# Kernel tuning notes

Measured on AMD Instinct MI355X. Metric: run time of the kernel, lower is better.

## Reference

```python
import jax, jax.numpy as jnp
import numpy as np

EMB = 1024
HEADS = 16
HEADSIZE = EMB // HEADS
EPS = 1e-5  # torch LayerNorm default


def _layernorm(x, g, b):
    # normalize over last dim (headsize)
    m = jnp.mean(x, axis=-1, keepdims=True)
    v = jnp.mean((x - m) ** 2, axis=-1, keepdims=True)
    return (x - m) * jax.lax.rsqrt(v + EPS) * g + b


def setup_inputs() -> dict:
    key = jax.random.key(0)
    ks = jax.random.split(key, 6)
    B, T = 4, 2048
    s = 1.0 / np.sqrt(EMB)  # ~ torch Linear init scale
    return {
        "x": jax.random.normal(ks[0], (B, T, EMB), dtype=jnp.float32),
        "Wk": jax.random.normal(ks[1], (EMB, EMB), dtype=jnp.float32) * s,
        "Wq": jax.random.normal(ks[2], (EMB, EMB), dtype=jnp.float32) * s,
        "Wv": jax.random.normal(ks[3], (EMB, EMB), dtype=jnp.float32) * s,
        "Wo": jax.random.normal(ks[4], (EMB, EMB), dtype=jnp.float32) * s,
        "bo": jnp.zeros((EMB,), dtype=jnp.float32),
        "kln_g": jnp.ones((HEADSIZE,), dtype=jnp.float32),
        "kln_b": jnp.zeros((HEADSIZE,), dtype=jnp.float32),
        "qln_g": jnp.ones((HEADSIZE,), dtype=jnp.float32),
        "qln_b": jnp.zeros((HEADSIZE,), dtype=jnp.float32),
    }


def reference(x, Wk, Wq, Wv, Wo, bo, kln_g, kln_b, qln_g, qln_b):
    B, T, E = x.shape
    # projections (torch Linear: y = x @ W.T), split into heads
    k = jnp.einsum("bte,fe->btf", x, Wk).reshape(B, T, HEADS, HEADSIZE)
    q = jnp.einsum("bte,fe->btf", x, Wq).reshape(B, T, HEADS, HEADSIZE)
    v = jnp.einsum("bte,fe->btf", x, Wv).reshape(B, T, HEADS, HEADSIZE)
    # optional per-head layernorm on keys/queries (kqnorm=True)
    k = _layernorm(k, kln_g, kln_b)
    q = _layernorm(q, qln_g, qln_b)
    # note: original scales by emb**-1/4 on each of q and k (total 1/sqrt(emb))
    scale = E ** (-0.25)
    q = q * scale
    k = k * scale
    # full [B, H, T, T] score matrix (faithful to bmm implementation)
    dot = jnp.einsum("bihd,bjhd->bhij", q, k)
    # causal mask: j > i set to -inf (mask_diagonal=False -> offset=1)
    causal = jnp.triu(jnp.ones((T, T), dtype=bool), k=1)
    dot = jnp.where(causal, -jnp.inf, dot)
    att = jax.nn.softmax(dot, axis=-1)
    out = jnp.einsum("bhij,bjhd->bihd", att, v).reshape(B, T, E)
    return jnp.einsum("bte,fe->btf", out, Wo) + bo
```

## Files before the change

### kernel.cpp

```cpp
#include <hip/hip_runtime.h>
#include <hip/hip_bf16.h>
#include <cstdint>

#define EMB 1024
#define HEADS 16
#define HD 64
#define BATCH 4
#define SEQ 2048
#define BT (BATCH*SEQ)
#define LNEPS 1e-5f
#define QK_SCALE 0.17677669529663687f
#define LOG2E 1.4426950408889634f

typedef __bf16 bf16;
typedef __bf16 bf16x8 __attribute__((ext_vector_type(8)));
typedef __bf16 bf16x4 __attribute__((ext_vector_type(4)));
typedef float  f32x4  __attribute__((ext_vector_type(4)));
typedef short  s16x4  __attribute__((ext_vector_type(4)));

typedef const __attribute__((address_space(1))) void* gas_ptr;
typedef __attribute__((address_space(3))) void*       las_ptr;

__device__ __forceinline__ void gld_lds16(const void* g, void* l) {
  __builtin_amdgcn_global_load_lds((gas_ptr)g, (las_ptr)l, 16, 0, 0);
}

__device__ __forceinline__ f32x4 mfma_pv(bf16x4 a, bf16x4 b, f32x4 c) {
  return __builtin_amdgcn_mfma_f32_16x16x16bf16_1k(
      __builtin_bit_cast(s16x4, a), __builtin_bit_cast(s16x4, b), c, 0, 0, 0);
}

__global__ void cvt_f32_bf16(const float* __restrict__ src, bf16* __restrict__ dst, int n4) {
  int i = blockIdx.x * blockDim.x + threadIdx.x;
  if (i >= n4) return;
  float4 f = reinterpret_cast<const float4*>(src)[i];
  bf16x4 o = { (bf16)f.x, (bf16)f.y, (bf16)f.z, (bf16)f.w };
  reinterpret_cast<bf16x4*>(dst)[i] = o;
}

__global__ void cvt_w4(const float* __restrict__ w0, const float* __restrict__ w1,
                       const float* __restrict__ w2, const float* __restrict__ w3,
                       bf16* __restrict__ dst) {
  int i = blockIdx.x * blockDim.x + threadIdx.x;
  int sel = i >> 18;
  int j = i & 262143;
  const float* s = (sel == 0) ? w0 : (sel == 1) ? w1 : (sel == 2) ? w2 : w3;
  float4 f = reinterpret_cast<const float4*>(s)[j];
  bf16x4 o = { (bf16)f.x, (bf16)f.y, (bf16)f.z, (bf16)f.w };
  reinterpret_cast<bf16x4*>(dst)[i] = o;
}

template<int OUTF32>
__global__ __launch_bounds__(256, 2) void gemm_bt(
    const bf16* __restrict__ A, const bf16* __restrict__ Bm,
    bf16* __restrict__ Cb, float* __restrict__ Cf, const float* __restrict__ bias,
    int M, int N, int K)
{
  __shared__ __align__(16) bf16 As[128 * 32];
  __shared__ __align__(16) bf16 Bs[128 * 32];

  const int t    = threadIdx.x;
  const int lane = t & 63;
  const int wave = t >> 6;
  const int q    = lane >> 4;
  const int ln   = lane & 15;
  const int m0   = blockIdx.y * 128;
  const int n0   = blockIdx.x * 128;
  const int wm   = (wave >> 1) * 64;
  const int wn   = (wave & 1) * 64;

  const int r0 = t >> 2;
  const int c0 = (t & 3) << 3;

  f32x4 zero4 = {0.f, 0.f, 0.f, 0.f};
  f32x4 acc[4][4];
#pragma unroll
  for (int i = 0; i < 4; i++)
#pragma unroll
    for (int j = 0; j < 4; j++) acc[i][j] = zero4;

  for (int k0 = 0; k0 < K; k0 += 32) {
    __syncthreads();
    const bf16* ga = A  + (size_t)(m0 + r0) * K + k0 + c0;
    const bf16* gb = Bm + (size_t)(n0 + r0) * K + k0 + c0;
    gld_lds16(ga,                  &As[t * 8]);
    gld_lds16(ga + (size_t)64 * K, &As[t * 8 + 2048]);
    gld_lds16(gb,                  &Bs[t * 8]);
    gld_lds16(gb + (size_t)64 * K, &Bs[t * 8 + 2048]);
    __syncthreads();

    bf16x8 af[4], bfr[4];
#pragma unroll
    for (int mi = 0; mi < 4; mi++)
      af[mi] = *reinterpret_cast<const bf16x8*>(&As[(wm + mi * 16 + ln) * 32 + q * 8]);
#pragma unroll
    for (int ni = 0; ni < 4; ni++)
      bfr[ni] = *reinterpret_cast<const bf16x8*>(&Bs[(wn + ni * 16 + ln) * 32 + q * 8]);
#pragma unroll
    for (int mi = 0; mi < 4; mi++)
#pragma unroll
      for (int ni = 0; ni < 4; ni++)
        acc[mi][ni] = __builtin_amdgcn_mfma_f32_16x16x32_bf16(af[mi], bfr[ni], acc[mi][ni], 0, 0, 0);
  }

#pragma unroll
  for (int mi = 0; mi < 4; mi++) {
#pragma unroll
    for (int ni = 0; ni < 4; ni++) {
#pragma unroll
      for (int r = 0; r < 4; r++) {
        int row = m0 + wm + mi * 16 + q * 4 + r;
        int col = n0 + wn + ni * 16 + ln;
        float v = acc[mi][ni][r];
        if (OUTF32) Cf[(size_t)row * N + col] = v + bias[col];
        else        Cb[(size_t)row * N + col] = (bf16)v;
      }
    }
  }
}

__global__ void ln_kq(const bf16* __restrict__ kqv,
                      bf16* __restrict__ kn, bf16* __restrict__ qn,
                      const float* __restrict__ kg, const float* __restrict__ kb,
                      const float* __restrict__ qg, const float* __restrict__ qb,
                      float kscale, float qscale)
{
  const int t = threadIdx.x;
  const int lr = t & 7;
  const int row = blockIdx.x * 32 + (t >> 3);
  const int tok = row >> 4, h = row & 15;
  const size_t base = (size_t)tok * (3 * EMB) + h * HD + lr * 8;

  bf16x8 vk = *reinterpret_cast<const bf16x8*>(kqv + base);
  bf16x8 vq = *reinterpret_cast<const bf16x8*>(kqv + base + EMB);

  float fk[8], fq[8];
  float sk = 0.f, sq = 0.f, s2k = 0.f, s2q = 0.f;
#pragma unroll
  for (int e = 0; e < 8; e++) {
    fk[e] = (float)vk[e]; fq[e] = (float)vq[e];
    sk += fk[e]; sq += fq[e];
    s2k += fk[e] * fk[e]; s2q += fq[e] * fq[e];
  }
#pragma unroll
  for (int m = 1; m < 8; m <<= 1) {
    sk  += __shfl_xor(sk,  m, 64); sq  += __shfl_xor(sq,  m, 64);
    s2k += __shfl_xor(s2k, m, 64); s2q += __shfl_xor(s2q, m, 64);
  }
  float mk = sk * (1.f / 64.f), mq = sq * (1.f / 64.f);
  float rk = rsqrtf(s2k * (1.f / 64.f) - mk * mk + LNEPS) * kscale;
  float rq = rsqrtf(s2q * (1.f / 64.f) - mq * mq + LNEPS) * qscale;

  bf16x8 ok, oq;
#pragma unroll
  for (int e = 0; e < 8; e++) {
    float gk = kg[lr * 8 + e], bk2 = kb[lr * 8 + e];
    float gq = qg[lr * 8 + e], bq2 = qb[lr * 8 + e];
    ok[e] = (bf16)(((fk[e] - mk) * rk) * gk + bk2 * kscale);
    oq[e] = (bf16)(((fq[e] - mq) * rq) * gq + bq2 * qscale);
  }
  const int b = tok >> 11, tt = tok & 2047;
  const size_t o = ((size_t)(b * HEADS + h) * SEQ + tt) * HD + lr * 8;
  *reinterpret_cast<bf16x8*>(kn + o) = ok;
  *reinterpret_cast<bf16x8*>(qn + o) = oq;
}

__global__ void v_trans(const bf16* __restrict__ in, int ldin, bf16* __restrict__ out)
{
  __shared__ __align__(16) bf16 tile[64][72];
  int bh = blockIdx.y, jt = blockIdx.x;
  int b = bh >> 4, h = bh & 15;
  int t = threadIdx.x;
#pragma unroll
  for (int p = 0; p < 2; p++) {
    int rowj = p * 32 + (t >> 3);
    int cold = (t & 7) << 3;
    bf16x8 v = *reinterpret_cast<const bf16x8*>(
        &in[(size_t)(b * SEQ + jt * 64 + rowj) * ldin + h * HD + cold]);
    *reinterpret_cast<bf16x8*>(&tile[rowj][cold]) = v;
  }
  __syncthreads();
#pragma unroll
  for (int p = 0; p < 2; p++) {
    int rowd = p * 32 + (t >> 3);
    int colj = (t & 7) << 3;
    bf16x8 v;
#pragma unroll
    for (int jj = 0; jj < 8; jj++) v[jj] = tile[colj + jj][rowd];
    *reinterpret_cast<bf16x8*>(&out[((size_t)bh * HD + rowd) * SEQ + jt * 64 + colj]) = v;
  }
}

__global__ __launch_bounds__(128, 8) void attn(
    const bf16* __restrict__ Qn, const bf16* __restrict__ Kn, const bf16* __restrict__ Vt,
    bf16* __restrict__ O)
{
  __shared__ __align__(16) bf16 Ks[32 * 64];
  __shared__ __align__(16) bf16 Vs[64 * 32];

  const int bh = blockIdx.y;
  const int itile = ((int)blockIdx.x + (int)blockIdx.y) & 63;
  const int i0 = itile * 32;
  const int t = threadIdx.x, wave = t >> 6, lane = t & 63;
  const int q = lane >> 4, ln = lane & 15;
  const int qbase = i0 + wave * 16;

  const bf16* qp = Qn + ((size_t)bh * SEQ + qbase + ln) * HD + q * 8;
  bf16x8 qf0 = *reinterpret_cast<const bf16x8*>(qp);
  bf16x8 qf1 = *reinterpret_cast<const bf16x8*>(qp + 32);

  float lrow = 0.f;
  f32x4 zero4 = {0.f, 0.f, 0.f, 0.f};
  f32x4 oacc[4];
#pragma unroll
  for (int md = 0; md < 4; md++) oacc[md] = zero4;

  const int nj = itile + 1;
  for (int jt = 0; jt < nj; jt++) {
    const int j0 = jt * 32;
#pragma unroll
    for (int s = 0; s < 2; s++) {
      int u = t * 8 + s * 1024;
      int krow = u >> 6;
      int kcs = ((u >> 3) & 7) ^ (krow & 7);
      gld_lds16(Kn + ((size_t)bh * SEQ + j0 + krow) * HD + kcs * 8, &Ks[u]);
      int vd = u >> 5;
      int vcs = ((u >> 3) & 3) ^ (vd & 3);
      gld_lds16(Vt + ((size_t)bh * HD + vd) * SEQ + j0 + vcs * 8, &Vs[u]);
    }
    __syncthreads();

#pragma unroll
    for (int jb = 0; jb < 2; jb++) {
      if ((j0 + jb * 16) <= (qbase + 15)) {
        const int rowj = jb * 16 + ln;
        bf16x8 kf0 = *reinterpret_cast<const bf16x8*>(&Ks[rowj * 64 + ((q)     ^ (rowj & 7)) * 8]);
        bf16x8 kf1 = *reinterpret_cast<const bf16x8*>(&Ks[rowj * 64 + ((4 + q) ^ (rowj & 7)) * 8]);
        f32x4 z = zero4;
        z = __builtin_amdgcn_mfma_f32_16x16x32_bf16(kf0, qf0, z, 0, 0, 0);
        z = __builtin_amdgcn_mfma_f32_16x16x32_bf16(kf1, qf1, z, 0, 0, 0);
        if (j0 + jb * 16 + 15 > qbase) {
#pragma unroll
          for (int r = 0; r < 4; r++) {
            int jj = j0 + jb * 16 + q * 4 + r;
            int ii = qbase + ln;
            if (jj > ii) z[r] = -1.0e30f;
          }
        }
        float p0 = exp2f(z[0]), p1 = exp2f(z[1]), p2 = exp2f(z[2]), p3 = exp2f(z[3]);
        lrow += (p0 + p1) + (p2 + p3);
        bf16x4 pk = { (bf16)p0, (bf16)p1, (bf16)p2, (bf16)p3 };

#pragma unroll
        for (int md = 0; md < 4; md++) {
          const int rowd = md * 16 + ln;
          const bf16* vp = &Vs[rowd * 32 + (((jb * 2 + (q >> 1)) ^ (rowd & 3)) * 8) + (q & 1) * 4];
          bf16x4 vf = *reinterpret_cast<const bf16x4*>(vp);
          oacc[md] = mfma_pv(vf, pk, oacc[md]);
        }
      }
    }
    __syncthreads();
  }

  float s = lrow;
  s += __shfl_xor(s, 16, 64);
  s += __shfl_xor(s, 32, 64);
  const float inv = 1.f / s;
  const int b = bh >> 4, h = bh & 15;
  const int row = qbase + ln;
#pragma unroll
  for (int md = 0; md < 4; md++) {
    bf16x4 o4 = { (bf16)(oacc[md][0] * inv), (bf16)(oacc[md][1] * inv),
                  (bf16)(oacc[md][2] * inv), (bf16)(oacc[md][3] * inv) };
    int col = h * HD + md * 16 + q * 4;
    *reinterpret_cast<bf16x4*>(&O[(size_t)(b * SEQ + row) * EMB + col]) = o4;
  }
}

extern "C" void kernel_launch(void* const* d_in, const int* in_sizes, int n_in,
                              void* d_out, int out_size, void* d_ws, size_t ws_size,
                              hipStream_t stream)
{
  const float* x   = (const float*)d_in[0];
  const float* Wk  = (const float*)d_in[1];
  const float* Wq  = (const float*)d_in[2];
  const float* Wv  = (const float*)d_in[3];
  const float* Wo  = (const float*)d_in[4];
  const float* bo  = (const float*)d_in[5];
  const float* klg = (const float*)d_in[6];
  const float* klb = (const float*)d_in[7];
  const float* qlg = (const float*)d_in[8];
  const float* qlb = (const float*)d_in[9];
  float* out = (float*)d_out;

  char* ws = (char*)d_ws;
  const size_t OFF_XB  = 0;
  const size_t OFF_WB  = OFF_XB  + (size_t)BT * EMB * 2;
  const size_t OFF_KQV = OFF_WB  + (size_t)4 * EMB * EMB * 2;
  const size_t OFF_KN  = OFF_KQV + (size_t)BT * 3 * EMB * 2;
  const size_t OFF_QN  = OFF_KN  + (size_t)BT * EMB * 2;
  const size_t OFF_VT  = OFF_QN  + (size_t)BT * EMB * 2;
  const size_t OFF_END = OFF_VT  + (size_t)BT * EMB * 2;
  if (ws_size < OFF_END) return;

  bf16* xb   = (bf16*)(ws + OFF_XB);
  bf16* wb   = (bf16*)(ws + OFF_WB);
  bf16* kqv  = (bf16*)(ws + OFF_KQV);
  bf16* kn   = (bf16*)(ws + OFF_KN);
  bf16* qn   = (bf16*)(ws + OFF_QN);
  bf16* vt   = (bf16*)(ws + OFF_VT);
  bf16* ob   = (bf16*)(ws + OFF_KQV);

  cvt_f32_bf16<<<(BT * EMB / 4) / 256, 256, 0, stream>>>(x, xb, BT * EMB / 4);
  cvt_w4<<<(4 * EMB * EMB / 4) / 256, 256, 0, stream>>>(Wk, Wq, Wv, Wo, wb);

  gemm_bt<0><<<dim3(3 * EMB / 128, BT / 128), 256, 0, stream>>>(
      xb, wb, kqv, (float*)nullptr, (const float*)nullptr, BT, 3 * EMB, EMB);

  ln_kq<<<BT * HEADS / 32, 256, 0, stream>>>(kqv, kn, qn, klg, klb, qlg, qlb,
                                             QK_SCALE * LOG2E, QK_SCALE);
  v_trans<<<dim3(SEQ / 64, BATCH * HEADS), 256, 0, stream>>>(kqv + 2 * EMB, 3 * EMB, vt);

  attn<<<dim3(64, BATCH * HEADS), 128, 0, stream>>>(qn, kn, vt, ob);

  gemm_bt<1><<<dim3(EMB / 128, BT / 128), 256, 0, stream>>>(
      ob, wb + (size_t)3 * EMB * EMB, (bf16*)nullptr, out, bo, BT, EMB, EMB);
}
```

Before: 316.8 us.

## Double query rows per attention wave to reuse K/V tiles across two strips

Each attention block now handles 64 query rows instead of 32, with each wave processing two 16-row strips that share the same K fragments and V fragment loads from LDS. This halves the number of blocks and the K/V global-to-LDS traffic per query row, and amortizes LDS reads over twice the MFMA work. The V LDS swizzle is also changed to reduce bank conflicts. The cost is higher register pressure (launch bounds lowered to 4 waves/SIMD occupancy hint), fewer blocks for load balancing across the causal triangle, and more wasted work on partially masked tiles.

```diff
diff --git a/kernel.cpp b/kernel.cpp
--- a/kernel.cpp
+++ b/kernel.cpp
@@ -191,7 +191,7 @@
   }
 }
 
-__global__ __launch_bounds__(128, 8) void attn(
+__global__ __launch_bounds__(128, 4) void attn(
     const bf16* __restrict__ Qn, const bf16* __restrict__ Kn, const bf16* __restrict__ Vt,
     bf16* __restrict__ O)
 {
@@ -199,23 +199,29 @@
   __shared__ __align__(16) bf16 Vs[64 * 32];
 
   const int bh = blockIdx.y;
-  const int itile = ((int)blockIdx.x + (int)blockIdx.y) & 63;
-  const int i0 = itile * 32;
+  const int itile = ((int)blockIdx.x + (int)blockIdx.y) & 31;
+  const int i0 = itile * 64;
   const int t = threadIdx.x, wave = t >> 6, lane = t & 63;
   const int q = lane >> 4, ln = lane & 15;
-  const int qbase = i0 + wave * 16;
-
-  const bf16* qp = Qn + ((size_t)bh * SEQ + qbase + ln) * HD + q * 8;
-  bf16x8 qf0 = *reinterpret_cast<const bf16x8*>(qp);
-  bf16x8 qf1 = *reinterpret_cast<const bf16x8*>(qp + 32);
-
-  float lrow = 0.f;
+  const int qbase = i0 + wave * 32;
+
+  bf16x8 qf[2][2];
+#pragma unroll
+  for (int it = 0; it < 2; it++) {
+    const bf16* qp = Qn + ((size_t)bh * SEQ + qbase + it * 16 + ln) * HD + q * 8;
+    qf[it][0] = *reinterpret_cast<const bf16x8*>(qp);
+    qf[it][1] = *reinterpret_cast<const bf16x8*>(qp + 32);
+  }
+
+  float lrow[2] = {0.f, 0.f};
   f32x4 zero4 = {0.f, 0.f, 0.f, 0.f};
-  f32x4 oacc[4];
-#pragma unroll
-  for (int md = 0; md < 4; md++) oacc[md] = zero4;
-
-  const int nj = itile + 1;
+  f32x4 oacc[4][2];
+#pragma unroll
+  for (int md = 0; md < 4; md++)
+#pragma unroll
+    for (int it = 0; it < 2; it++) oacc[md][it] = zero4;
+
+  const int nj = 2 * (itile + 1);
   for (int jt = 0; jt < nj; jt++) {
     const int j0 = jt * 32;
 #pragma unroll
@@ -225,57 +231,72 @@
       int kcs = ((u >> 3) & 7) ^ (krow & 7);
       gld_lds16(Kn + ((size_t)bh * SEQ + j0 + krow) * HD + kcs * 8, &Ks[u]);
       int vd = u >> 5;
-      int vcs = ((u >> 3) & 3) ^ (vd & 3);
+      int vcs = ((u >> 3) & 3) ^ ((vd >> 1) & 3);
       gld_lds16(Vt + ((size_t)bh * HD + vd) * SEQ + j0 + vcs * 8, &Vs[u]);
     }
     __syncthreads();
 
 #pragma unroll
     for (int jb = 0; jb < 2; jb++) {
-      if ((j0 + jb * 16) <= (qbase + 15)) {
-        const int rowj = jb * 16 + ln;
-        bf16x8 kf0 = *reinterpret_cast<const bf16x8*>(&Ks[rowj * 64 + ((q)     ^ (rowj & 7)) * 8]);
-        bf16x8 kf1 = *reinterpret_cast<const bf16x8*>(&Ks[rowj * 64 + ((4 + q) ^ (rowj & 7)) * 8]);
+      const int rowj = jb * 16 + ln;
+      bf16x8 kf0 = *reinterpret_cast<const bf16x8*>(&Ks[rowj * 64 + ((q)     ^ (rowj & 7)) * 8]);
+      bf16x8 kf1 = *reinterpret_cast<const bf16x8*>(&Ks[rowj * 64 + ((4 + q) ^ (rowj & 7)) * 8]);
+
+      bf16x4 pkf[2];
+      bool live[2];
+#pragma unroll
+      for (int it = 0; it < 2; it++) {
+        live[it] = (j0 + jb * 16) <= (qbase + it * 16 + 15);
+        if (!live[it]) continue;
         f32x4 z = zero4;
-        z = __builtin_amdgcn_mfma_f32_16x16x32_bf16(kf0, qf0, z, 0, 0, 0);
-        z = __builtin_amdgcn_mfma_f32_16x16x32_bf16(kf1, qf1, z, 0, 0, 0);
-        if (j0 + jb * 16 + 15 > qbase) {
+        z = __builtin_amdgcn_mfma_f32_16x16x32_bf16(kf0, qf[it][0], z, 0, 0, 0);
+        z = __builtin_amdgcn_mfma_f32_16x16x32_bf16(kf1, qf[it][1], z, 0, 0, 0);
+        if (j0 + jb * 16 + 15 > qbase + it * 16) {
 #pragma unroll
           for (int r = 0; r < 4; r++) {
             int jj = j0 + jb * 16 + q * 4 + r;
-            int ii = qbase + ln;
+            int ii = qbase + it * 16 + ln;
             if (jj > ii) z[r] = -1.0e30f;
           }
         }
         float p0 = exp2f(z[0]), p1 = exp2f(z[1]), p2 = exp2f(z[2]), p3 = exp2f(z[3]);
-        lrow += (p0 + p1) + (p2 + p3);
+        lrow[it] += (p0 + p1) + (p2 + p3);
         bf16x4 pk = { (bf16)p0, (bf16)p1, (bf16)p2, (bf16)p3 };
-
-#pragma unroll
-        for (int md = 0; md < 4; md++) {
-          const int rowd = md * 16 + ln;
-          const bf16* vp = &Vs[rowd * 32 + (((jb * 2 + (q >> 1)) ^ (rowd & 3)) * 8) + (q & 1) * 4];
-          bf16x4 vf = *reinterpret_cast<const bf16x4*>(vp);
-          oacc[md] = mfma_pv(vf, pk, oacc[md]);
-        }
+        pkf[it] = pk;
+      }
+
+#pragma unroll
+      for (int md = 0; md < 4; md++) {
+        const int rowd = md * 16 + ln;
+        const bf16* vp = &Vs[rowd * 32 + (((jb * 2 + (q >> 1)) ^ ((rowd >> 1) & 3)) * 8) + (q & 1) * 4];
+        bf16x4 vf = *reinterpret_cast<const bf16x4*>(vp);
+#pragma unroll
+        for (int it = 0; it < 2; it++)
+          if (live[it]) oacc[md][it] = mfma_pv(vf, pkf[it], oacc[md][it]);
       }
     }
     __syncthreads();
   }
 
-  float s = lrow;
-  s += __shfl_xor(s, 16, 64);
-  s += __shfl_xor(s, 32, 64);
-  const float inv = 1.f / s;
+  float inv[2];
+#pragma unroll
+  for (int it = 0; it < 2; it++) {
+    float s = lrow[it];
+    s += __shfl_xor(s, 16, 64);
+    s += __shfl_xor(s, 32, 64);
+    inv[it] = 1.f / s;
+  }
   const int b = bh >> 4, h = bh & 15;
-  const int row = qbase + ln;
-#pragma unroll
-  for (int md = 0; md < 4; md++) {
-    bf16x4 o4 = { (bf16)(oacc[md][0] * inv), (bf16)(oacc[md][1] * inv),
-                  (bf16)(oacc[md][2] * inv), (bf16)(oacc[md][3] * inv) };
-    int col = h * HD + md * 16 + q * 4;
-    *reinterpret_cast<bf16x4*>(&O[(size_t)(b * SEQ + row) * EMB + col]) = o4;
-  }
+#pragma unroll
+  for (int md = 0; md < 4; md++)
+#pragma unroll
+    for (int it = 0; it < 2; it++) {
+      bf16x4 o4 = { (bf16)(oacc[md][it][0] * inv[it]), (bf16)(oacc[md][it][1] * inv[it]),
+                    (bf16)(oacc[md][it][2] * inv[it]), (bf16)(oacc[md][it][3] * inv[it]) };
+      int row = qbase + it * 16 + ln;
+      int col = h * HD + md * 16 + q * 4;
+      *reinterpret_cast<bf16x4*>(&O[(size_t)(b * SEQ + row) * EMB + col]) = o4;
+    }
 }
 
 extern "C" void kernel_launch(void* const* d_in, const int* in_sizes, int n_in,
@@ -322,7 +343,7 @@
                                              QK_SCALE * LOG2E, QK_SCALE);
   v_trans<<<dim3(SEQ / 64, BATCH * HEADS), 256, 0, stream>>>(kqv + 2 * EMB, 3 * EMB, vt);
 
-  attn<<<dim3(64, BATCH * HEADS), 128, 0, stream>>>(qn, kn, vt, ob);
+  attn<<<dim3(32, BATCH * HEADS), 128, 0, stream>>>(qn, kn, vt, ob);
 
   gemm_bt<1><<<dim3(EMB / 128, BT / 128), 256, 0, stream>>>(
       ob, wb + (size_t)3 * EMB * EMB, (bf16*)nullptr, out, bo, BT, EMB, EMB);
```

Result: slower. 329.0 us (+3.9%).
